# Optimization experiments

Measured on AMD Instinct MI355X. Metric: run time of the kernel, lower is better.

The kernel has to match this reference:

```python
import jax, jax.numpy as jnp
import numpy as np

EPS = 1e-10


def setup_inputs() -> dict:
    key = jax.random.key(0)
    k_in, k_len, k_u, k_w, k_b, k_cb = jax.random.split(key, 6)
    B, S, D_in = 16, 4096, 512
    G, C, D_out = 2, 320, 256
    inputs = jax.random.normal(k_in, (B, S, D_in), dtype=jnp.float32)
    valid_lengths = jax.random.randint(k_len, (B,), 1, S + 1, dtype=jnp.int64)
    noise_u = jax.random.uniform(k_u, (B, S, G, C), dtype=jnp.float32)
    # projector params (nn.Linear default init scale is irrelevant for correctness)
    W = jax.random.normal(k_w, (G * C, D_in), dtype=jnp.float32) * (1.0 / np.sqrt(D_in))
    b = jax.random.normal(k_b, (G * C,), dtype=jnp.float32) * 0.01
    codebook = jax.random.uniform(k_cb, (G, C, D_out // G), dtype=jnp.float32,
                                  minval=-1.0 / C, maxval=1.0 / C)
    temperature = jnp.asarray(2.0, dtype=jnp.float32)
    return {"inputs": inputs, "valid_lengths": valid_lengths, "noise_u": noise_u,
            "W": W, "b": b, "codebook": codebook, "temperature": temperature}


def reference(inputs, valid_lengths, noise_u, W, b, codebook, temperature):
    B, S, _ = inputs.shape
    G, C, Dg = codebook.shape
    # dense projector GEMM: [B,S,Din] @ [Din,G*C]
    logits = (jnp.einsum('bsi,oi->bso', inputs, W) + b).reshape(B, S, G, C)
    # gumbel-softmax with straight-through hard selection (F.gumbel_softmax)
    gumbels = -jnp.log(-jnp.log(noise_u + EPS) + EPS)
    y_soft = jax.nn.softmax((logits + gumbels) / temperature, axis=-1)
    idx = jnp.argmax(y_soft, axis=-1)                       # [B,S,G]
    y_hard = jax.nn.one_hot(idx, C, dtype=y_soft.dtype)
    choice_probs = y_hard - jax.lax.stop_gradient(y_soft) + y_soft
    # masked usage stats over valid positions
    soft_probs = jax.nn.softmax(logits, axis=-1)            # [B,S,G,C]
    mask = (jnp.arange(S)[None, :] < valid_lengths[:, None]).astype(soft_probs.dtype)
    masked_sum = jnp.einsum('bsgc,bs->gc', soft_probs, mask)
    usage = masked_sum / jnp.sum(mask)
    # per-group codebook lookup via einsum against small table
    quantized = jnp.einsum('bsgc,gcd->bsgd', choice_probs, codebook).reshape(B, S, G * Dg)
    return quantized, usage
```

## Files before the change

### kernel.cpp

```cpp
#include <hip/hip_runtime.h>
#include <math.h>

#define NB 16
#define NS 4096
#define DIN 512
#define NG 2
#define NC 320
#define GC 640
#define DG 128
#define NROW (NB*NS)
#define NKT 16
#define NCT 40
#define EPSV 1e-10f

typedef __attribute__((ext_vector_type(4))) float f32x4;
typedef __attribute__((ext_vector_type(8))) _Float16 f16x8;

__device__ __forceinline__ void gload_lds16(const void* g, void* l) {
    __builtin_amdgcn_global_load_lds(
        (const __attribute__((address_space(1))) void*)g,
        (__attribute__((address_space(3))) void*)l,
        16, 0, 0);
}

__global__ __launch_bounds__(256) void cvt_split_pack(
    const float* __restrict__ W, _Float16* __restrict__ hp, _Float16* __restrict__ lp)
{
    int idx = blockIdx.x * 256 + threadIdx.x;
    if (idx >= GC * (DIN / 8)) return;
    int col = idx >> 6, k8 = idx & 63;
    int kslice = k8 >> 2, kq = k8 & 3, ntile = col >> 4;
    int ln = (col & 15) + 16 * kq;
    size_t dst = (((size_t)kslice * NCT + ntile) * 64 + ln) * 8;
    const float* src = W + (size_t)col * DIN + k8 * 8;
    f16x8 h, l;
    #pragma unroll
    for (int j = 0; j < 8; ++j) {
        float x = src[j];
        _Float16 hh = (_Float16)x;
        h[j] = hh;
        l[j] = (_Float16)((x - (float)hh) * 2048.0f);
    }
    *(f16x8*)(hp + dst) = h;
    *(f16x8*)(lp + dst) = l;
}

__global__ __launch_bounds__(512, 4) void mfma_logits3(
    const float* __restrict__ X,
    const _Float16* __restrict__ Whp, const _Float16* __restrict__ Wlp,
    const float* __restrict__ bias, float* __restrict__ logits)
{
    __shared__ _Float16 sA[2][2][128 * 32];

    const int t = threadIdx.x;
    const int lane = t & 63;
    const int w = t >> 6;
    const int wm = w >> 2, wn = w & 3;

    const int p = blockIdx.x;
    const int o = (p & 7) * 320 + (p >> 3);
    const int mb = o / 5, nb = o - mb * 5;
    const int row0 = mb * 128, n0 = nb * 128;
    const int ct0 = (n0 >> 4) + wn * 2;

    const int ar = t >> 2, aq = t & 3;
    const int aidx = ar * 32 + 8 * (aq ^ ((ar >> 1) & 3));
    const float* aga = X + (size_t)(row0 + ar) * DIN + 8 * aq;

    float4 a0, a1;
    auto loadA = [&](int k0) {
        a0 = ((const float4*)(aga + k0))[0];
        a1 = ((const float4*)(aga + k0))[1];
    };
    auto writeA = [&](int b) {
        float xs[8] = {a0.x, a0.y, a0.z, a0.w, a1.x, a1.y, a1.z, a1.w};
        f16x8 h, l;
        #pragma unroll
        for (int j = 0; j < 8; ++j) {
            _Float16 hh = (_Float16)xs[j];
            h[j] = hh;
            l[j] = (_Float16)((xs[j] - (float)hh) * 2048.0f);
        }
        *(f16x8*)&sA[b][0][aidx] = h;
        *(f16x8*)&sA[b][1][aidx] = l;
    };

    f32x4 accA[4][2], accB[4][2];
    const f32x4 zz = {0.f, 0.f, 0.f, 0.f};
    #pragma unroll
    for (int mt = 0; mt < 4; ++mt)
        #pragma unroll
        for (int nt = 0; nt < 2; ++nt) { accA[mt][nt] = zz; accB[mt][nt] = zz; }

    loadA(0);
    writeA(0);
    asm volatile("s_waitcnt lgkmcnt(0)" ::: "memory");
    __builtin_amdgcn_s_barrier();
    __builtin_amdgcn_sched_barrier(0);

    for (int ks = 0; ks < NKT; ++ks) {
        const int cur = ks & 1;
        if (ks < NKT - 1) loadA((ks + 1) * 32);

        f16x8 bh[2], bl[2];
        #pragma unroll
        for (int nt = 0; nt < 2; ++nt) {
            size_t off = (((size_t)ks * NCT) + ct0 + nt) * 64 + lane;
            bh[nt] = *(const f16x8*)(Whp + off * 8);
            bl[nt] = *(const f16x8*)(Wlp + off * 8);
        }
        f16x8 ah[4], al[4];
        #pragma unroll
        for (int mt = 0; mt < 4; ++mt) {
            int r = wm * 64 + mt * 16 + (lane & 15);
            int idx = r * 32 + 8 * ((lane >> 4) ^ ((r >> 1) & 3));
            ah[mt] = *(const f16x8*)&sA[cur][0][idx];
            al[mt] = *(const f16x8*)&sA[cur][1][idx];
        }
        #pragma unroll
        for (int mt = 0; mt < 4; ++mt)
            #pragma unroll
            for (int nt = 0; nt < 2; ++nt) {
                accA[mt][nt] = __builtin_amdgcn_mfma_f32_16x16x32_f16(ah[mt], bh[nt], accA[mt][nt], 0, 0, 0);
                accB[mt][nt] = __builtin_amdgcn_mfma_f32_16x16x32_f16(ah[mt], bl[nt], accB[mt][nt], 0, 0, 0);
                accB[mt][nt] = __builtin_amdgcn_mfma_f32_16x16x32_f16(al[mt], bh[nt], accB[mt][nt], 0, 0, 0);
            }

        if (ks < NKT - 1) {
            writeA(cur ^ 1);
            asm volatile("s_waitcnt lgkmcnt(0)" ::: "memory");
            __builtin_amdgcn_s_barrier();
            __builtin_amdgcn_sched_barrier(0);
        }
    }

    #pragma unroll
    for (int nt = 0; nt < 2; ++nt) {
        int col = n0 + wn * 32 + nt * 16 + (lane & 15);
        float bv = bias[col];
        #pragma unroll
        for (int mt = 0; mt < 4; ++mt) {
            #pragma unroll
            for (int q = 0; q < 4; ++q) {
                int row = row0 + wm * 64 + mt * 16 + (lane >> 4) * 4 + q;
                logits[(size_t)row * GC + col] =
                    accA[mt][nt][q] + accB[mt][nt][q] * (1.0f / 2048.0f) + bv;
            }
        }
    }
}

#define RTB 32
__global__ __launch_bounds__(256, 8) void epilogue(
    const float* __restrict__ logits, const int* __restrict__ vlen,
    const float* __restrict__ U, const float* __restrict__ CB,
    float* __restrict__ out, float* __restrict__ gacc)
{
    __shared__ float uacc[GC];
    const int t = threadIdx.x;
    const int lane = t & 63;
    const int wid = t >> 6;
    const int row0 = blockIdx.x * RTB;

    for (int i = t; i < GC; i += 256) uacc[i] = 0.0f;
    __syncthreads();

    const int vl = vlen[row0 >> 12];

    float ureg[10];
    #pragma unroll
    for (int j = 0; j < 10; ++j) ureg[j] = 0.0f;

    #pragma unroll
    for (int r = 0; r < 8; ++r) {
        const int row = row0 + wid * 8 + r;
        const bool valid = (row & (NS - 1)) < vl;

        float lg[10], zz[10];
        #pragma unroll
        for (int j = 0; j < 10; ++j)
            lg[j] = logits[(size_t)row * GC + lane + 64 * j];
        #pragma unroll
        for (int j = 0; j < 10; ++j) {
            float u = U[(size_t)row * GC + lane + 64 * j];
            zz[j] = lg[j] - logf(-logf(u + EPSV) + EPSV);
        }

        #pragma unroll
        for (int g = 0; g < 2; ++g) {
            const int j0 = g * 5;

            float mv = zz[j0];
            #pragma unroll
            for (int j = j0 + 1; j < j0 + 5; ++j) mv = fmaxf(mv, zz[j]);
            #pragma unroll
            for (int d = 1; d < 64; d <<= 1) mv = fmaxf(mv, __shfl_xor(mv, d));

            int c = 0;
            #pragma unroll
            for (int jj = 4; jj >= 0; --jj) {
                unsigned long long b = __ballot(zz[j0 + jj] == mv);
                if (b) c = (__ffsll(b) - 1) + 64 * jj;
            }

            float pe[5], s2 = 0.0f;
            #pragma unroll
            for (int jj = 0; jj < 5; ++jj) {
                pe[jj] = __expf(lg[j0 + jj]);
                s2 += pe[jj];
            }
            #pragma unroll
            for (int d = 1; d < 64; d <<= 1) s2 += __shfl_xor(s2, d);
            if (valid) {
                const float inv = 1.0f / s2;
                #pragma unroll
                for (int jj = 0; jj < 5; ++jj) ureg[j0 + jj] += pe[jj] * inv;
            }

            const float2 cv = ((const float2*)(CB + ((size_t)g * NC + c) * DG))[lane];
            ((float2*)(out + (size_t)row * (NG * DG) + g * DG))[lane] = cv;
        }
    }

    #pragma unroll
    for (int j = 0; j < 10; ++j)
        atomicAdd(&uacc[lane + 64 * j], ureg[j]);

    __syncthreads();
    for (int i = t; i < GC; i += 256) atomicAdd(&gacc[i], uacc[i]);
}

__global__ void finalize_usage(const float* __restrict__ gacc,
                               const int* __restrict__ vlen,
                               float* __restrict__ usage_out)
{
    int total = 0;
    #pragma unroll
    for (int b = 0; b < NB; ++b) total += vlen[b];
    int o = threadIdx.x;
    if (o < GC) usage_out[o] = gacc[o] / (float)total;
}

#define RT 32
#define KC 8
#define NIT (DIN/KC)

__global__ void transpose_w(const float* __restrict__ W, float* __restrict__ Wt) {
    int idx = blockIdx.x * 256 + threadIdx.x;
    if (idx >= GC * DIN) return;
    int k = idx / GC, o = idx - k * GC;
    Wt[idx] = W[(size_t)o * DIN + k];
}

__global__ __launch_bounds__(256, 2) void fused_main(
    const float* __restrict__ X, const int* __restrict__ vlen,
    const float* __restrict__ U, const float* __restrict__ Wt,
    const float* __restrict__ bias, const float* __restrict__ CB,
    const float* __restrict__ tptr, float* __restrict__ out,
    float* __restrict__ gacc)
{
    __shared__ __align__(16) float WtC[2][KC][GC];
    __shared__ __align__(16) float AC[2][RT][KC];
    __shared__ float uacc[GC];

    const int t = threadIdx.x;
    const int lane = t & 63;
    const int wid = t >> 6;
    const int row0 = blockIdx.x * RT;

    for (int i = t; i < GC; i += 256) uacc[i] = 0.0f;

    float acc[8][10];
    #pragma unroll
    for (int r = 0; r < 8; ++r)
        #pragma unroll
        for (int j = 0; j < 10; ++j) acc[r][j] = 0.0f;

    auto stage = [&](int b, int k0) {
        const float* gw = Wt + (size_t)k0 * GC;
        #pragma unroll
        for (int i = 0; i < 5; ++i) {
            int base = (wid * 5 + i) * 256;
            gload_lds16(gw + base + 4 * lane, &WtC[b][0][0] + base);
        }
        if (wid == 0) {
            const float* gx = X + (size_t)(row0 + (lane >> 1)) * DIN + k0 + 4 * (lane & 1);
            gload_lds16(gx, &AC[b][0][0]);
        }
    };

    stage(0, 0);
    __syncthreads();

    int cur = 0;
    for (int it = 0; it < NIT; ++it) {
        if (it + 1 < NIT) stage(cur ^ 1, (it + 1) * KC);
        #pragma unroll
        for (int kk = 0; kk < KC; ++kk) {
            float w[10];
            #pragma unroll
            for (int j = 0; j < 10; ++j) w[j] = WtC[cur][kk][lane + 64 * j];
            #pragma unroll
            for (int r = 0; r < 8; ++r) {
                float a = AC[cur][wid * 8 + r][kk];
                #pragma unroll
                for (int j = 0; j < 10; ++j) acc[r][j] = fmaf(a, w[j], acc[r][j]);
            }
        }
        __syncthreads();
        cur ^= 1;
    }

    float bv[10];
    #pragma unroll
    for (int j = 0; j < 10; ++j) bv[j] = bias[lane + 64 * j];
    #pragma unroll
    for (int r = 0; r < 8; ++r)
        #pragma unroll
        for (int j = 0; j < 10; ++j) acc[r][j] += bv[j];

    const float T = *tptr;
    const int vl = vlen[row0 >> 12];

    #pragma unroll
    for (int r = 0; r < 8; ++r) {
        const int row = row0 + wid * 8 + r;
        const int ss = row & (NS - 1);
        const bool valid = ss < vl;

        float z[10];
        #pragma unroll
        for (int j = 0; j < 10; ++j) {
            float u = U[(size_t)row * GC + lane + 64 * j];
            float gn = -logf(-logf(u + EPSV) + EPSV);
            z[j] = (acc[r][j] + gn) / T;
        }

        #pragma unroll
        for (int g = 0; g < 2; ++g) {
            const int j0 = g * 5;
            float mv = z[j0];
            int mo = lane + 64 * j0;
            #pragma unroll
            for (int j = j0 + 1; j < j0 + 5; ++j) {
                if (z[j] > mv) { mv = z[j]; mo = lane + 64 * j; }
            }
            #pragma unroll
            for (int d = 1; d < 64; d <<= 1) {
                float ov = __shfl_xor(mv, d);
                int   oo = __shfl_xor(mo, d);
                if (ov > mv || (ov == mv && oo < mo)) { mv = ov; mo = oo; }
            }
            float se = 0.0f;
            #pragma unroll
            for (int j = j0; j < j0 + 5; ++j) se += expf(z[j] - mv);
            #pragma unroll
            for (int d = 1; d < 64; d <<= 1) se += __shfl_xor(se, d);
            float y = 1.0f / se;
            float q = (1.0f - y) + y;

            float m2 = acc[r][j0];
            #pragma unroll
            for (int j = j0 + 1; j < j0 + 5; ++j) m2 = fmaxf(m2, acc[r][j]);
            #pragma unroll
            for (int d = 1; d < 64; d <<= 1) m2 = fmaxf(m2, __shfl_xor(m2, d));
            float pe[5];
            float s2 = 0.0f;
            #pragma unroll
            for (int jj = 0; jj < 5; ++jj) {
                pe[jj] = expf(acc[r][j0 + jj] - m2);
                s2 += pe[jj];
            }
            #pragma unroll
            for (int d = 1; d < 64; d <<= 1) s2 += __shfl_xor(s2, d);
            if (valid) {
                #pragma unroll
                for (int jj = 0; jj < 5; ++jj)
                    atomicAdd(&uacc[lane + 64 * (j0 + jj)], pe[jj] / s2);
            }

            const int c = mo - g * NC;
            const float2 cv = ((const float2*)(CB + ((size_t)g * NC + c) * DG))[lane];
            float2 ov2;
            ov2.x = q * cv.x;
            ov2.y = q * cv.y;
            ((float2*)(out + (size_t)row * (NG * DG) + g * DG))[lane] = ov2;
        }
    }

    __syncthreads();
    for (int i = t; i < GC; i += 256) atomicAdd(&gacc[i], uacc[i]);
}

extern "C" void kernel_launch(void* const* d_in, const int* in_sizes, int n_in,
                              void* d_out, int out_size, void* d_ws, size_t ws_size,
                              hipStream_t stream)
{
    const float* X    = (const float*)d_in[0];
    const int*   vlen = (const int*)d_in[1];
    const float* U    = (const float*)d_in[2];
    const float* W    = (const float*)d_in[3];
    const float* bias = (const float*)d_in[4];
    const float* CB   = (const float*)d_in[5];
    const float* T    = (const float*)d_in[6];
    float* out = (float*)d_out;

    char* ws = (char*)d_ws;
    float*     gacc = (float*)ws;
    _Float16*  Whp  = (_Float16*)(ws + 4096);
    _Float16*  Wlp  = (_Float16*)(ws + 659456);
    float*     lgts = (float*)(ws + 1314816);
    float*     Wt   = (float*)(ws + 4096);
    const size_t need = 1314816ull + 167772160ull;

    hipMemsetAsync(gacc, 0, GC * sizeof(float), stream);

    if (ws_size >= need) {
        cvt_split_pack<<<(GC * (DIN / 8) + 255) / 256, 256, 0, stream>>>(W, Whp, Wlp);
        mfma_logits3<<<(NROW / 128) * 5, 512, 0, stream>>>(X, Whp, Wlp, bias, lgts);
        epilogue<<<NROW / RTB, 256, 0, stream>>>(lgts, vlen, U, CB, out, gacc);
    } else {
        transpose_w<<<(GC * DIN + 255) / 256, 256, 0, stream>>>(W, Wt);
        fused_main<<<NROW / RT, 256, 0, stream>>>(X, vlen, U, Wt, bias, CB, T, out, gacc);
    }
    finalize_usage<<<1, GC, 0, stream>>>(gacc, vlen, out + (size_t)NROW * (NG * DG));
}
```

Measured before the change: 272.3 us.

## Fuse MFMA logits GEMM with gumbel argmax/usage epilogue per 64-row tile

Replaces the separate GEMM kernel (which wrote a 168MB fp32 logits buffer) and the epilogue kernel with one kernel. Each block computes all 640 columns for 64 rows, one group at a time, and does the gumbel argmax, softmax sums and usage accumulation from registers through small shared-memory cross-wave reductions. This removes the logits write and re-read through global memory. In exchange the block re-reads X once per group, has a smaller M-tile with more B loads per MFMA, and adds extra barriers.

```diff
diff --git a/kernel.cpp b/kernel.cpp
--- a/kernel.cpp
+++ b/kernel.cpp
@@ -15,6 +15,7 @@
 
 typedef __attribute__((ext_vector_type(4))) float f32x4;
 typedef __attribute__((ext_vector_type(8))) _Float16 f16x8;
+typedef __attribute__((ext_vector_type(4))) _Float16 f16x4v;
 
 __device__ __forceinline__ void gload_lds16(const void* g, void* l) {
     __builtin_amdgcn_global_load_lds(
@@ -45,12 +46,19 @@
     *(f16x8*)(lp + dst) = l;
 }
 
-__global__ __launch_bounds__(512, 4) void mfma_logits3(
-    const float* __restrict__ X,
+__global__ __launch_bounds__(512, 2) void fused_mfma(
+    const float* __restrict__ X, const int* __restrict__ vlen,
+    const float* __restrict__ U,
     const _Float16* __restrict__ Whp, const _Float16* __restrict__ Wlp,
-    const float* __restrict__ bias, float* __restrict__ logits)
+    const float* __restrict__ bias, const float* __restrict__ CB,
+    float* __restrict__ out, float* __restrict__ gacc)
 {
-    __shared__ _Float16 sA[2][2][128 * 32];
+    __shared__ _Float16 sA[2][2][64 * 32];
+    __shared__ float pmaxS[64][4];
+    __shared__ int   pcolS[64][4];
+    __shared__ float psumS[64][4];
+    __shared__ float invsS[64];
+    __shared__ float uacc[NC];
 
     const int t = threadIdx.x;
     const int lane = t & 63;
@@ -58,176 +66,159 @@
     const int wm = w >> 2, wn = w & 3;
 
     const int p = blockIdx.x;
-    const int o = (p & 7) * 320 + (p >> 3);
-    const int mb = o / 5, nb = o - mb * 5;
-    const int row0 = mb * 128, n0 = nb * 128;
-    const int ct0 = (n0 >> 4) + wn * 2;
-
-    const int ar = t >> 2, aq = t & 3;
-    const int aidx = ar * 32 + 8 * (aq ^ ((ar >> 1) & 3));
-    const float* aga = X + (size_t)(row0 + ar) * DIN + 8 * aq;
-
-    float4 a0, a1;
-    auto loadA = [&](int k0) {
-        a0 = ((const float4*)(aga + k0))[0];
-        a1 = ((const float4*)(aga + k0))[1];
-    };
+    const int bo = (p & 7) * 128 + (p >> 3);
+    const int row0 = bo * 64;
+    const int vl = vlen[row0 >> 12];
+
+    const int ar = t >> 3, kq = (t >> 1) & 3, half = t & 1;
+    const int aidx = ar * 32 + 8 * (kq ^ ((ar >> 1) & 3)) + 4 * half;
+    const float* aga = X + (size_t)(row0 + ar) * DIN + 8 * kq + 4 * half;
+
+    float4 a0;
     auto writeA = [&](int b) {
-        float xs[8] = {a0.x, a0.y, a0.z, a0.w, a1.x, a1.y, a1.z, a1.w};
-        f16x8 h, l;
-        #pragma unroll
-        for (int j = 0; j < 8; ++j) {
+        float xs[4] = {a0.x, a0.y, a0.z, a0.w};
+        f16x4v h, l;
+        #pragma unroll
+        for (int j = 0; j < 4; ++j) {
             _Float16 hh = (_Float16)xs[j];
             h[j] = hh;
             l[j] = (_Float16)((xs[j] - (float)hh) * 2048.0f);
         }
-        *(f16x8*)&sA[b][0][aidx] = h;
-        *(f16x8*)&sA[b][1][aidx] = l;
+        *(f16x4v*)&sA[b][0][aidx] = h;
+        *(f16x4v*)&sA[b][1][aidx] = l;
     };
 
-    f32x4 accA[4][2], accB[4][2];
-    const f32x4 zz = {0.f, 0.f, 0.f, 0.f};
-    #pragma unroll
-    for (int mt = 0; mt < 4; ++mt)
-        #pragma unroll
-        for (int nt = 0; nt < 2; ++nt) { accA[mt][nt] = zz; accB[mt][nt] = zz; }
-
-    loadA(0);
-    writeA(0);
-    asm volatile("s_waitcnt lgkmcnt(0)" ::: "memory");
-    __builtin_amdgcn_s_barrier();
-    __builtin_amdgcn_sched_barrier(0);
-
-    for (int ks = 0; ks < NKT; ++ks) {
-        const int cur = ks & 1;
-        if (ks < NKT - 1) loadA((ks + 1) * 32);
-
-        f16x8 bh[2], bl[2];
-        #pragma unroll
-        for (int nt = 0; nt < 2; ++nt) {
-            size_t off = (((size_t)ks * NCT) + ct0 + nt) * 64 + lane;
-            bh[nt] = *(const f16x8*)(Whp + off * 8);
-            bl[nt] = *(const f16x8*)(Wlp + off * 8);
-        }
-        f16x8 ah[4], al[4];
-        #pragma unroll
-        for (int mt = 0; mt < 4; ++mt) {
-            int r = wm * 64 + mt * 16 + (lane & 15);
-            int idx = r * 32 + 8 * ((lane >> 4) ^ ((r >> 1) & 3));
-            ah[mt] = *(const f16x8*)&sA[cur][0][idx];
-            al[mt] = *(const f16x8*)&sA[cur][1][idx];
-        }
-        #pragma unroll
-        for (int mt = 0; mt < 4; ++mt)
-            #pragma unroll
-            for (int nt = 0; nt < 2; ++nt) {
-                accA[mt][nt] = __builtin_amdgcn_mfma_f32_16x16x32_f16(ah[mt], bh[nt], accA[mt][nt], 0, 0, 0);
-                accB[mt][nt] = __builtin_amdgcn_mfma_f32_16x16x32_f16(ah[mt], bl[nt], accB[mt][nt], 0, 0, 0);
-                accB[mt][nt] = __builtin_amdgcn_mfma_f32_16x16x32_f16(al[mt], bh[nt], accB[mt][nt], 0, 0, 0);
-            }
-
-        if (ks < NKT - 1) {
-            writeA(cur ^ 1);
-            asm volatile("s_waitcnt lgkmcnt(0)" ::: "memory");
-            __builtin_amdgcn_s_barrier();
-            __builtin_amdgcn_sched_barrier(0);
-        }
+    #pragma unroll 1
+    for (int g = 0; g < 2; ++g) {
+        if (t < NC) uacc[t] = 0.0f;
+
+        f32x4 accA[2][5], accB[2][5];
+        const f32x4 zz4 = {0.f, 0.f, 0.f, 0.f};
+        #pragma unroll
+        for (int mt = 0; mt < 2; ++mt)
+            #pragma unroll
+            for (int nt = 0; nt < 5; ++nt) { accA[mt][nt] = zz4; accB[mt][nt] = zz4; }
+
+        a0 = *(const float4*)(aga);
+        writeA(0);
+        asm volatile("s_waitcnt lgkmcnt(0)" ::: "memory");
+        __builtin_amdgcn_s_barrier();
+
+        for (int ks = 0; ks < NKT; ++ks) {
+            const int cur = ks & 1;
+            if (ks < NKT - 1) a0 = *(const float4*)(aga + (ks + 1) * 32);
+
+            f16x8 bh[5], bl[5];
+            #pragma unroll
+            for (int nt = 0; nt < 5; ++nt) {
+                size_t off = ((size_t)ks * NCT + g * 20 + wn * 5 + nt) * 64 + lane;
+                bh[nt] = *(const f16x8*)(Whp + off * 8);
+                bl[nt] = *(const f16x8*)(Wlp + off * 8);
+            }
+            f16x8 ah[2], al[2];
+            #pragma unroll
+            for (int mt = 0; mt < 2; ++mt) {
+                int r = wm * 32 + mt * 16 + (lane & 15);
+                int idx = r * 32 + 8 * ((lane >> 4) ^ ((r >> 1) & 3));
+                ah[mt] = *(const f16x8*)&sA[cur][0][idx];
+                al[mt] = *(const f16x8*)&sA[cur][1][idx];
+            }
+            #pragma unroll
+            for (int mt = 0; mt < 2; ++mt)
+                #pragma unroll
+                for (int nt = 0; nt < 5; ++nt) {
+                    accA[mt][nt] = __builtin_amdgcn_mfma_f32_16x16x32_f16(ah[mt], bh[nt], accA[mt][nt], 0, 0, 0);
+                    accB[mt][nt] = __builtin_amdgcn_mfma_f32_16x16x32_f16(ah[mt], bl[nt], accB[mt][nt], 0, 0, 0);
+                    accB[mt][nt] = __builtin_amdgcn_mfma_f32_16x16x32_f16(al[mt], bh[nt], accB[mt][nt], 0, 0, 0);
+                }
+
+            if (ks < NKT - 1) {
+                writeA(cur ^ 1);
+                asm volatile("s_waitcnt lgkmcnt(0)" ::: "memory");
+                __builtin_amdgcn_s_barrier();
+            }
+        }
+
+        float bv[5];
+        #pragma unroll
+        for (int nt = 0; nt < 5; ++nt)
+            bv[nt] = bias[g * 320 + wn * 80 + nt * 16 + (lane & 15)];
+        f32x4 lg[2][5];
+        #pragma unroll
+        for (int mt = 0; mt < 2; ++mt)
+            #pragma unroll
+            for (int nt = 0; nt < 5; ++nt)
+                #pragma unroll
+                for (int q = 0; q < 4; ++q)
+                    lg[mt][nt][q] = accA[mt][nt][q] + accB[mt][nt][q] * (1.0f / 2048.0f) + bv[nt];
+
+        const int colbase = wn * 80 + (lane & 15);
+        #pragma unroll
+        for (int mt = 0; mt < 2; ++mt)
+            #pragma unroll
+            for (int q = 0; q < 4; ++q) {
+                const int rl = wm * 32 + mt * 16 + (lane >> 4) * 4 + q;
+                const int row = row0 + rl;
+                float bestv = -3.4e38f; int bestc = 0;
+                float s2 = 0.0f;
+                #pragma unroll
+                for (int nt = 0; nt < 5; ++nt) {
+                    float lgv = lg[mt][nt][q];
+                    float u = U[(size_t)row * GC + g * 320 + colbase + nt * 16];
+                    float znt = lgv - logf(-logf(u + EPSV) + EPSV);
+                    int cc = colbase + nt * 16;
+                    if (znt > bestv) { bestv = znt; bestc = cc; }
+                    s2 += __expf(lgv);
+                }
+                #pragma unroll
+                for (int d = 1; d < 16; d <<= 1) {
+                    float ov = __shfl_xor(bestv, d);
+                    int   oc = __shfl_xor(bestc, d);
+                    if (ov > bestv || (ov == bestv && oc < bestc)) { bestv = ov; bestc = oc; }
+                    s2 += __shfl_xor(s2, d);
+                }
+                if ((lane & 15) == 0) {
+                    pmaxS[rl][wn] = bestv; pcolS[rl][wn] = bestc; psumS[rl][wn] = s2;
+                }
+            }
+        __syncthreads();
+
+        {
+            const int r = t >> 3, j = t & 7;
+            float bvv = pmaxS[r][0]; int bc = pcolS[r][0];
+            float s2 = psumS[r][0];
+            #pragma unroll
+            for (int wv = 1; wv < 4; ++wv) {
+                float v = pmaxS[r][wv]; int c = pcolS[r][wv];
+                if (v > bvv || (v == bvv && c < bc)) { bvv = v; bc = c; }
+                s2 += psumS[r][wv];
+            }
+            if (j == 0) invsS[r] = 1.0f / s2;
+            const float4* src = (const float4*)(CB + ((size_t)g * NC + bc) * DG + j * 16);
+            float4* dst = (float4*)(out + (size_t)(row0 + r) * (NG * DG) + g * DG + j * 16);
+            dst[0] = src[0]; dst[1] = src[1]; dst[2] = src[2]; dst[3] = src[3];
+        }
+        __syncthreads();
+
+        float ureg[5] = {0.f, 0.f, 0.f, 0.f, 0.f};
+        #pragma unroll
+        for (int mt = 0; mt < 2; ++mt)
+            #pragma unroll
+            for (int q = 0; q < 4; ++q) {
+                const int rl = wm * 32 + mt * 16 + (lane >> 4) * 4 + q;
+                if (((row0 + rl) & (NS - 1)) < vl) {
+                    float inv = invsS[rl];
+                    #pragma unroll
+                    for (int nt = 0; nt < 5; ++nt)
+                        ureg[nt] += __expf(lg[mt][nt][q]) * inv;
+                }
+            }
+        #pragma unroll
+        for (int nt = 0; nt < 5; ++nt)
+            atomicAdd(&uacc[colbase + nt * 16], ureg[nt]);
+        __syncthreads();
+        if (t < NC) atomicAdd(&gacc[g * NC + t], uacc[t]);
     }
-
-    #pragma unroll
-    for (int nt = 0; nt < 2; ++nt) {
-        int col = n0 + wn * 32 + nt * 16 + (lane & 15);
-        float bv = bias[col];
-        #pragma unroll
-        for (int mt = 0; mt < 4; ++mt) {
-            #pragma unroll
-            for (int q = 0; q < 4; ++q) {
-                int row = row0 + wm * 64 + mt * 16 + (lane >> 4) * 4 + q;
-                logits[(size_t)row * GC + col] =
-                    accA[mt][nt][q] + accB[mt][nt][q] * (1.0f / 2048.0f) + bv;
-            }
-        }
-    }
-}
-
-#define RTB 32
-__global__ __launch_bounds__(256, 8) void epilogue(
-    const float* __restrict__ logits, const int* __restrict__ vlen,
-    const float* __restrict__ U, const float* __restrict__ CB,
-    float* __restrict__ out, float* __restrict__ gacc)
-{
-    __shared__ float uacc[GC];
-    const int t = threadIdx.x;
-    const int lane = t & 63;
-    const int wid = t >> 6;
-    const int row0 = blockIdx.x * RTB;
-
-    for (int i = t; i < GC; i += 256) uacc[i] = 0.0f;
-    __syncthreads();
-
-    const int vl = vlen[row0 >> 12];
-
-    float ureg[10];
-    #pragma unroll
-    for (int j = 0; j < 10; ++j) ureg[j] = 0.0f;
-
-    #pragma unroll
-    for (int r = 0; r < 8; ++r) {
-        const int row = row0 + wid * 8 + r;
-        const bool valid = (row & (NS - 1)) < vl;
-
-        float lg[10], zz[10];
-        #pragma unroll
-        for (int j = 0; j < 10; ++j)
-            lg[j] = logits[(size_t)row * GC + lane + 64 * j];
-        #pragma unroll
-        for (int j = 0; j < 10; ++j) {
-            float u = U[(size_t)row * GC + lane + 64 * j];
-            zz[j] = lg[j] - logf(-logf(u + EPSV) + EPSV);
-        }
-
-        #pragma unroll
-        for (int g = 0; g < 2; ++g) {
-            const int j0 = g * 5;
-
-            float mv = zz[j0];
-            #pragma unroll
-            for (int j = j0 + 1; j < j0 + 5; ++j) mv = fmaxf(mv, zz[j]);
-            #pragma unroll
-            for (int d = 1; d < 64; d <<= 1) mv = fmaxf(mv, __shfl_xor(mv, d));
-
-            int c = 0;
-            #pragma unroll
-            for (int jj = 4; jj >= 0; --jj) {
-                unsigned long long b = __ballot(zz[j0 + jj] == mv);
-                if (b) c = (__ffsll(b) - 1) + 64 * jj;
-            }
-
-            float pe[5], s2 = 0.0f;
-            #pragma unroll
-            for (int jj = 0; jj < 5; ++jj) {
-                pe[jj] = __expf(lg[j0 + jj]);
-                s2 += pe[jj];
-            }
-            #pragma unroll
-            for (int d = 1; d < 64; d <<= 1) s2 += __shfl_xor(s2, d);
-            if (valid) {
-                const float inv = 1.0f / s2;
-                #pragma unroll
-                for (int jj = 0; jj < 5; ++jj) ureg[j0 + jj] += pe[jj] * inv;
-            }
-
-            const float2 cv = ((const float2*)(CB + ((size_t)g * NC + c) * DG))[lane];
-            ((float2*)(out + (size_t)row * (NG * DG) + g * DG))[lane] = cv;
-        }
-    }
-
-    #pragma unroll
-    for (int j = 0; j < 10; ++j)
-        atomicAdd(&uacc[lane + 64 * j], ureg[j]);
-
-    __syncthreads();
-    for (int i = t; i < GC; i += 256) atomicAdd(&gacc[i], uacc[i]);
 }
 
 __global__ void finalize_usage(const float* __restrict__ gacc,
@@ -297,14 +288,14 @@
         if (it + 1 < NIT) stage(cur ^ 1, (it + 1) * KC);
         #pragma unroll
         for (int kk = 0; kk < KC; ++kk) {
-            float w[10];
-            #pragma unroll
-            for (int j = 0; j < 10; ++j) w[j] = WtC[cur][kk][lane + 64 * j];
+            float wv[10];
+            #pragma unroll
+            for (int j = 0; j < 10; ++j) wv[j] = WtC[cur][kk][lane + 64 * j];
             #pragma unroll
             for (int r = 0; r < 8; ++r) {
                 float a = AC[cur][wid * 8 + r][kk];
                 #pragma unroll
-                for (int j = 0; j < 10; ++j) acc[r][j] = fmaf(a, w[j], acc[r][j]);
+                for (int j = 0; j < 10; ++j) acc[r][j] = fmaf(a, wv[j], acc[r][j]);
             }
         }
         __syncthreads();
@@ -409,16 +400,14 @@
     float*     gacc = (float*)ws;
     _Float16*  Whp  = (_Float16*)(ws + 4096);
     _Float16*  Wlp  = (_Float16*)(ws + 659456);
-    float*     lgts = (float*)(ws + 1314816);
     float*     Wt   = (float*)(ws + 4096);
-    const size_t need = 1314816ull + 167772160ull;
+    const size_t need = 4096ull + 2ull * 655360ull;
 
     hipMemsetAsync(gacc, 0, GC * sizeof(float), stream);
 
     if (ws_size >= need) {
         cvt_split_pack<<<(GC * (DIN / 8) + 255) / 256, 256, 0, stream>>>(W, Whp, Wlp);
-        mfma_logits3<<<(NROW / 128) * 5, 512, 0, stream>>>(X, Whp, Wlp, bias, lgts);
-        epilogue<<<NROW / RTB, 256, 0, stream>>>(lgts, vlen, U, CB, out, gacc);
+        fused_mfma<<<NROW / 64, 512, 0, stream>>>(X, vlen, U, Whp, Wlp, bias, CB, out, gacc);
     } else {
         transpose_w<<<(GC * DIN + 255) / 256, 256, 0, stream>>>(W, Wt);
         fused_main<<<NROW / RT, 256, 0, stream>>>(X, vlen, U, Wt, bias, CB, T, out, gacc);
```

Result: slower. 349.2 us (+28.2%).

## Enlarge MFMA GEMM block tile to 256 rows with 64-column warp tiles

Applied to the files above, without the earlier changes.

The split-fp16 MFMA logits kernel now processes 256 rows per block instead of 128, and each wave covers 64 rows by 64 columns instead of 64 by 32. This halves the number of blocks and doubles reuse of the B fragments and the converted A tile per wave, cutting global reads of W and per-block overhead. In exchange it doubles accumulator registers and LDS per block, so occupancy drops to 2 blocks per CU. The explicit sched_barriers were also removed, which changes how the compiler may schedule instructions.

```diff
diff --git a/kernel.cpp b/kernel.cpp
--- a/kernel.cpp
+++ b/kernel.cpp
@@ -45,67 +45,85 @@
     *(f16x8*)(lp + dst) = l;
 }
 
-__global__ __launch_bounds__(512, 4) void mfma_logits3(
+__global__ __launch_bounds__(512, 2) void mfma_logits4(
     const float* __restrict__ X,
     const _Float16* __restrict__ Whp, const _Float16* __restrict__ Wlp,
     const float* __restrict__ bias, float* __restrict__ logits)
 {
-    __shared__ _Float16 sA[2][2][128 * 32];
+    __shared__ _Float16 sA[2][2][256 * 32];
 
     const int t = threadIdx.x;
     const int lane = t & 63;
     const int w = t >> 6;
-    const int wm = w >> 2, wn = w & 3;
+    const int wm = w >> 1, wn = w & 1;
 
     const int p = blockIdx.x;
-    const int o = (p & 7) * 320 + (p >> 3);
-    const int mb = o / 5, nb = o - mb * 5;
-    const int row0 = mb * 128, n0 = nb * 128;
-    const int ct0 = (n0 >> 4) + wn * 2;
+    const int bo = (p & 7) * 160 + (p >> 3);
+    const int mb = bo / 5, nb = bo - mb * 5;
+    const int row0 = mb * 256, n0 = nb * 128;
+    const int ct0 = nb * 8 + wn * 4;
 
     const int ar = t >> 2, aq = t & 3;
-    const int aidx = ar * 32 + 8 * (aq ^ ((ar >> 1) & 3));
-    const float* aga = X + (size_t)(row0 + ar) * DIN + 8 * aq;
-
-    float4 a0, a1;
+    const int sw = aq ^ ((ar >> 1) & 3);
+    const int aidx0 = ar * 32 + 8 * sw;
+    const int aidx1 = (ar + 128) * 32 + 8 * sw;
+    const float* aga0 = X + (size_t)(row0 + ar) * DIN + 8 * aq;
+    const float* aga1 = X + (size_t)(row0 + 128 + ar) * DIN + 8 * aq;
+
+    float4 a0, a1, a2, a3;
     auto loadA = [&](int k0) {
-        a0 = ((const float4*)(aga + k0))[0];
-        a1 = ((const float4*)(aga + k0))[1];
+        a0 = ((const float4*)(aga0 + k0))[0];
+        a1 = ((const float4*)(aga0 + k0))[1];
+        a2 = ((const float4*)(aga1 + k0))[0];
+        a3 = ((const float4*)(aga1 + k0))[1];
     };
     auto writeA = [&](int b) {
-        float xs[8] = {a0.x, a0.y, a0.z, a0.w, a1.x, a1.y, a1.z, a1.w};
-        f16x8 h, l;
-        #pragma unroll
-        for (int j = 0; j < 8; ++j) {
-            _Float16 hh = (_Float16)xs[j];
-            h[j] = hh;
-            l[j] = (_Float16)((xs[j] - (float)hh) * 2048.0f);
-        }
-        *(f16x8*)&sA[b][0][aidx] = h;
-        *(f16x8*)&sA[b][1][aidx] = l;
+        {
+            float xs[8] = {a0.x, a0.y, a0.z, a0.w, a1.x, a1.y, a1.z, a1.w};
+            f16x8 h, l;
+            #pragma unroll
+            for (int j = 0; j < 8; ++j) {
+                _Float16 hh = (_Float16)xs[j];
+                h[j] = hh;
+                l[j] = (_Float16)((xs[j] - (float)hh) * 2048.0f);
+            }
+            *(f16x8*)&sA[b][0][aidx0] = h;
+            *(f16x8*)&sA[b][1][aidx0] = l;
+        }
+        {
+            float xs[8] = {a2.x, a2.y, a2.z, a2.w, a3.x, a3.y, a3.z, a3.w};
+            f16x8 h, l;
+            #pragma unroll
+            for (int j = 0; j < 8; ++j) {
+                _Float16 hh = (_Float16)xs[j];
+                h[j] = hh;
+                l[j] = (_Float16)((xs[j] - (float)hh) * 2048.0f);
+            }
+            *(f16x8*)&sA[b][0][aidx1] = h;
+            *(f16x8*)&sA[b][1][aidx1] = l;
+        }
     };
 
-    f32x4 accA[4][2], accB[4][2];
+    f32x4 accA[4][4], accB[4][4];
     const f32x4 zz = {0.f, 0.f, 0.f, 0.f};
     #pragma unroll
     for (int mt = 0; mt < 4; ++mt)
         #pragma unroll
-        for (int nt = 0; nt < 2; ++nt) { accA[mt][nt] = zz; accB[mt][nt] = zz; }
+        for (int nt = 0; nt < 4; ++nt) { accA[mt][nt] = zz; accB[mt][nt] = zz; }
 
     loadA(0);
     writeA(0);
     asm volatile("s_waitcnt lgkmcnt(0)" ::: "memory");
     __builtin_amdgcn_s_barrier();
-    __builtin_amdgcn_sched_barrier(0);
 
     for (int ks = 0; ks < NKT; ++ks) {
         const int cur = ks & 1;
         if (ks < NKT - 1) loadA((ks + 1) * 32);
 
-        f16x8 bh[2], bl[2];
-        #pragma unroll
-        for (int nt = 0; nt < 2; ++nt) {
-            size_t off = (((size_t)ks * NCT) + ct0 + nt) * 64 + lane;
+        f16x8 bh[4], bl[4];
+        #pragma unroll
+        for (int nt = 0; nt < 4; ++nt) {
+            size_t off = ((size_t)ks * NCT + ct0 + nt) * 64 + lane;
             bh[nt] = *(const f16x8*)(Whp + off * 8);
             bl[nt] = *(const f16x8*)(Wlp + off * 8);
         }
@@ -120,7 +138,7 @@
         #pragma unroll
         for (int mt = 0; mt < 4; ++mt)
             #pragma unroll
-            for (int nt = 0; nt < 2; ++nt) {
+            for (int nt = 0; nt < 4; ++nt) {
                 accA[mt][nt] = __builtin_amdgcn_mfma_f32_16x16x32_f16(ah[mt], bh[nt], accA[mt][nt], 0, 0, 0);
                 accB[mt][nt] = __builtin_amdgcn_mfma_f32_16x16x32_f16(ah[mt], bl[nt], accB[mt][nt], 0, 0, 0);
                 accB[mt][nt] = __builtin_amdgcn_mfma_f32_16x16x32_f16(al[mt], bh[nt], accB[mt][nt], 0, 0, 0);
@@ -130,13 +148,12 @@
             writeA(cur ^ 1);
             asm volatile("s_waitcnt lgkmcnt(0)" ::: "memory");
             __builtin_amdgcn_s_barrier();
-            __builtin_amdgcn_sched_barrier(0);
-        }
-    }
-
-    #pragma unroll
-    for (int nt = 0; nt < 2; ++nt) {
-        int col = n0 + wn * 32 + nt * 16 + (lane & 15);
+        }
+    }
+
+    #pragma unroll
+    for (int nt = 0; nt < 4; ++nt) {
+        int col = n0 + wn * 64 + nt * 16 + (lane & 15);
         float bv = bias[col];
         #pragma unroll
         for (int mt = 0; mt < 4; ++mt) {
@@ -297,14 +314,14 @@
         if (it + 1 < NIT) stage(cur ^ 1, (it + 1) * KC);
         #pragma unroll
         for (int kk = 0; kk < KC; ++kk) {
-            float w[10];
-            #pragma unroll
-            for (int j = 0; j < 10; ++j) w[j] = WtC[cur][kk][lane + 64 * j];
+            float wv[10];
+            #pragma unroll
+            for (int j = 0; j < 10; ++j) wv[j] = WtC[cur][kk][lane + 64 * j];
             #pragma unroll
             for (int r = 0; r < 8; ++r) {
                 float a = AC[cur][wid * 8 + r][kk];
                 #pragma unroll
-                for (int j = 0; j < 10; ++j) acc[r][j] = fmaf(a, w[j], acc[r][j]);
+                for (int j = 0; j < 10; ++j) acc[r][j] = fmaf(a, wv[j], acc[r][j]);
             }
         }
         __syncthreads();
@@ -417,7 +434,7 @@
 
     if (ws_size >= need) {
         cvt_split_pack<<<(GC * (DIN / 8) + 255) / 256, 256, 0, stream>>>(W, Whp, Wlp);
-        mfma_logits3<<<(NROW / 128) * 5, 512, 0, stream>>>(X, Whp, Wlp, bias, lgts);
+        mfma_logits4<<<(NROW / 256) * 5, 512, 0, stream>>>(X, Whp, Wlp, bias, lgts);
         epilogue<<<NROW / RTB, 256, 0, stream>>>(lgts, vlen, U, CB, out, gacc);
     } else {
         transpose_w<<<(GC * DIN + 255) / 256, 256, 0, stream>>>(W, Wt);
```

Measured after the change: 285.2 us. 1.05x slower.

## Pre-split activations into packed fp16 hi/lo buffers and use LDS-free MFMA GEMM

Applied to the files above, without the earlier changes.

Adds a separate pass that converts the fp32 activations into MFMA-fragment-packed fp16 high/low halves in workspace. A new GEMM kernel then loads both A and B fragments directly from global memory, with no LDS staging or barriers, on 128x64 tiles with 256 threads. The aim is to take the per-block fp32-to-fp16 split and LDS synchronisation out of the GEMM. The cost is an extra 134 MB of workspace traffic and a larger workspace requirement, with the old path kept as a fallback. It also drops sched_barrier hints in the old kernel.

```diff
diff --git a/kernel.cpp b/kernel.cpp
--- a/kernel.cpp
+++ b/kernel.cpp
@@ -45,6 +45,94 @@
     *(f16x8*)(lp + dst) = l;
 }
 
+__global__ __launch_bounds__(256) void cvt_split_packA(
+    const float* __restrict__ X, _Float16* __restrict__ hp, _Float16* __restrict__ lp)
+{
+    int idx = blockIdx.x * 256 + threadIdx.x;
+    int row = idx >> 6, k8 = idx & 63;
+    int ks = k8 >> 2, kq = k8 & 3;
+    int rt = row >> 4, rl = row & 15;
+    size_t dst = (((size_t)rt * NKT + ks) * 64 + (rl + 16 * kq)) * 8;
+    const float* src = X + (size_t)row * DIN + k8 * 8;
+    float4 v0 = ((const float4*)src)[0];
+    float4 v1 = ((const float4*)src)[1];
+    float xs[8] = {v0.x, v0.y, v0.z, v0.w, v1.x, v1.y, v1.z, v1.w};
+    f16x8 h, l;
+    #pragma unroll
+    for (int j = 0; j < 8; ++j) {
+        _Float16 hh = (_Float16)xs[j];
+        h[j] = hh;
+        l[j] = (_Float16)((xs[j] - (float)hh) * 2048.0f);
+    }
+    *(f16x8*)(hp + dst) = h;
+    *(f16x8*)(lp + dst) = l;
+}
+
+__global__ __launch_bounds__(256, 3) void mfma_logits5(
+    const _Float16* __restrict__ Ahp, const _Float16* __restrict__ Alp,
+    const _Float16* __restrict__ Whp, const _Float16* __restrict__ Wlp,
+    const float* __restrict__ bias, float* __restrict__ logits)
+{
+    const int t = threadIdx.x;
+    const int lane = t & 63;
+    const int w = t >> 6;
+    const int wm = w >> 1, wn = w & 1;
+
+    const int p = blockIdx.x;
+    const int bo = (p & 7) * 640 + (p >> 3);
+    const int mb = bo / 10, nbk = bo - mb * 10;
+    const int row0 = mb * 128, n0 = nbk * 64;
+    const int ct0 = nbk * 4 + wn * 2;
+    const int rt0 = (row0 >> 4) + wm * 4;
+
+    f32x4 accA[4][2], accB[4][2];
+    const f32x4 zz = {0.f, 0.f, 0.f, 0.f};
+    #pragma unroll
+    for (int mt = 0; mt < 4; ++mt)
+        #pragma unroll
+        for (int nt = 0; nt < 2; ++nt) { accA[mt][nt] = zz; accB[mt][nt] = zz; }
+
+    #pragma unroll
+    for (int ks = 0; ks < NKT; ++ks) {
+        f16x8 ah[4], al[4], bh[2], bl[2];
+        #pragma unroll
+        for (int mt = 0; mt < 4; ++mt) {
+            size_t aoff = (((size_t)(rt0 + mt) * NKT + ks) * 64 + lane) * 8;
+            ah[mt] = *(const f16x8*)(Ahp + aoff);
+            al[mt] = *(const f16x8*)(Alp + aoff);
+        }
+        #pragma unroll
+        for (int nt = 0; nt < 2; ++nt) {
+            size_t boff = (((size_t)ks * NCT) + ct0 + nt) * 64 + lane;
+            bh[nt] = *(const f16x8*)(Whp + boff * 8);
+            bl[nt] = *(const f16x8*)(Wlp + boff * 8);
+        }
+        #pragma unroll
+        for (int mt = 0; mt < 4; ++mt)
+            #pragma unroll
+            for (int nt = 0; nt < 2; ++nt) {
+                accA[mt][nt] = __builtin_amdgcn_mfma_f32_16x16x32_f16(ah[mt], bh[nt], accA[mt][nt], 0, 0, 0);
+                accB[mt][nt] = __builtin_amdgcn_mfma_f32_16x16x32_f16(ah[mt], bl[nt], accB[mt][nt], 0, 0, 0);
+                accB[mt][nt] = __builtin_amdgcn_mfma_f32_16x16x32_f16(al[mt], bh[nt], accB[mt][nt], 0, 0, 0);
+            }
+    }
+
+    #pragma unroll
+    for (int nt = 0; nt < 2; ++nt) {
+        int col = n0 + wn * 32 + nt * 16 + (lane & 15);
+        float bv = bias[col];
+        #pragma unroll
+        for (int mt = 0; mt < 4; ++mt) {
+            #pragma unroll
+            for (int q = 0; q < 4; ++q) {
+                int row = row0 + wm * 64 + mt * 16 + (lane >> 4) * 4 + q;
+                logits[(size_t)row * GC + col] =
+                    accA[mt][nt][q] + accB[mt][nt][q] * (1.0f / 2048.0f) + bv;
+            }
+        }
+    }
+}
+
 __global__ __launch_bounds__(512, 4) void mfma_logits3(
     const float* __restrict__ X,
     const _Float16* __restrict__ Whp, const _Float16* __restrict__ Wlp,
@@ -96,7 +184,6 @@
     writeA(0);
     asm volatile("s_waitcnt lgkmcnt(0)" ::: "memory");
     __builtin_amdgcn_s_barrier();
-    __builtin_amdgcn_sched_barrier(0);
 
     for (int ks = 0; ks < NKT; ++ks) {
         const int cur = ks & 1;
@@ -130,7 +217,6 @@
             writeA(cur ^ 1);
             asm volatile("s_waitcnt lgkmcnt(0)" ::: "memory");
             __builtin_amdgcn_s_barrier();
-            __builtin_amdgcn_sched_barrier(0);
         }
     }
 
@@ -297,14 +383,14 @@
         if (it + 1 < NIT) stage(cur ^ 1, (it + 1) * KC);
         #pragma unroll
         for (int kk = 0; kk < KC; ++kk) {
-            float w[10];
-            #pragma unroll
-            for (int j = 0; j < 10; ++j) w[j] = WtC[cur][kk][lane + 64 * j];
+            float wv[10];
+            #pragma unroll
+            for (int j = 0; j < 10; ++j) wv[j] = WtC[cur][kk][lane + 64 * j];
             #pragma unroll
             for (int r = 0; r < 8; ++r) {
                 float a = AC[cur][wid * 8 + r][kk];
                 #pragma unroll
-                for (int j = 0; j < 10; ++j) acc[r][j] = fmaf(a, w[j], acc[r][j]);
+                for (int j = 0; j < 10; ++j) acc[r][j] = fmaf(a, wv[j], acc[r][j]);
             }
         }
         __syncthreads();
@@ -409,16 +495,25 @@
     float*     gacc = (float*)ws;
     _Float16*  Whp  = (_Float16*)(ws + 4096);
     _Float16*  Wlp  = (_Float16*)(ws + 659456);
-    float*     lgts = (float*)(ws + 1314816);
+    _Float16*  Ahp  = (_Float16*)(ws + 1314816);
+    _Float16*  Alp  = (_Float16*)(ws + 68423680);
+    float*     lgtsA = (float*)(ws + 135532544);
+    float*     lgtsM = (float*)(ws + 1314816);
     float*     Wt   = (float*)(ws + 4096);
-    const size_t need = 1314816ull + 167772160ull;
+    const size_t need_big = 135532544ull + 167772160ull;
+    const size_t need_mid = 1314816ull + 167772160ull;
 
     hipMemsetAsync(gacc, 0, GC * sizeof(float), stream);
 
-    if (ws_size >= need) {
+    if (ws_size >= need_big) {
         cvt_split_pack<<<(GC * (DIN / 8) + 255) / 256, 256, 0, stream>>>(W, Whp, Wlp);
-        mfma_logits3<<<(NROW / 128) * 5, 512, 0, stream>>>(X, Whp, Wlp, bias, lgts);
-        epilogue<<<NROW / RTB, 256, 0, stream>>>(lgts, vlen, U, CB, out, gacc);
+        cvt_split_packA<<<NROW * 64 / 256, 256, 0, stream>>>(X, Ahp, Alp);
+        mfma_logits5<<<(NROW / 128) * 10, 256, 0, stream>>>(Ahp, Alp, Whp, Wlp, bias, lgtsA);
+        epilogue<<<NROW / RTB, 256, 0, stream>>>(lgtsA, vlen, U, CB, out, gacc);
+    } else if (ws_size >= need_mid) {
+        cvt_split_pack<<<(GC * (DIN / 8) + 255) / 256, 256, 0, stream>>>(W, Whp, Wlp);
+        mfma_logits3<<<(NROW / 128) * 5, 512, 0, stream>>>(X, Whp, Wlp, bias, lgtsM);
+        epilogue<<<NROW / RTB, 256, 0, stream>>>(lgtsM, vlen, U, CB, out, gacc);
     } else {
         transpose_w<<<(GC * DIN + 255) / 256, 256, 0, stream>>>(W, Wt);
         fused_main<<<NROW / RT, 256, 0, stream>>>(X, vlen, U, Wt, bias, CB, T, out, gacc);
```

New measurement: 562.3 us. 2.06x slower.
